# Kernel tuning notes

Hardware: AMD Instinct MI355X
Metric: run time of the kernel (lower is better)

## Reference

```python
import jax, jax.numpy as jnp
import numpy as np

N_E = 1024
N_H = 16
SZ = N_E // N_H  # 64
NEG_INF = float('-inf')


def _layernorm(x, g, b):
    # Faithful to source: unbiased variance (ddof=1), eps added AFTER sqrt.
    mu = jnp.mean(x, axis=-1, keepdims=True)
    v = jnp.var(x, axis=-1, keepdims=True, ddof=1)
    xn = (x - mu) / (jnp.sqrt(v) + 1e-8)
    return g * xn + b


def setup_inputs() -> dict:
    key = jax.random.key(0)
    ks = jax.random.split(key, 16)
    s = 0.02
    x = jax.random.normal(ks[0], (4, 2048, N_E), dtype=jnp.float32)
    # Stacked per-head Q/K/V linears: weight [H, sz, n_e], bias [H, sz]
    Wq = jax.random.normal(ks[1], (N_H, SZ, N_E), dtype=jnp.float32) * s
    bq = jax.random.normal(ks[2], (N_H, SZ), dtype=jnp.float32) * s
    Wk = jax.random.normal(ks[3], (N_H, SZ, N_E), dtype=jnp.float32) * s
    bk = jax.random.normal(ks[4], (N_H, SZ), dtype=jnp.float32) * s
    Wv = jax.random.normal(ks[5], (N_H, SZ, N_E), dtype=jnp.float32) * s
    bv = jax.random.normal(ks[6], (N_H, SZ), dtype=jnp.float32) * s
    Wo = jax.random.normal(ks[7], (N_E, N_E), dtype=jnp.float32) * s
    bo = jax.random.normal(ks[8], (N_E,), dtype=jnp.float32) * s
    g1 = jnp.ones((N_E,), dtype=jnp.float32)
    be1 = jnp.zeros((N_E,), dtype=jnp.float32)
    g2 = jnp.ones((N_E,), dtype=jnp.float32)
    be2 = jnp.zeros((N_E,), dtype=jnp.float32)
    W1 = jax.random.normal(ks[9], (4 * N_E, N_E), dtype=jnp.float32) * s
    bf1 = jax.random.normal(ks[10], (4 * N_E,), dtype=jnp.float32) * s
    W2 = jax.random.normal(ks[11], (N_E, 4 * N_E), dtype=jnp.float32) * s
    bf2 = jax.random.normal(ks[12], (N_E,), dtype=jnp.float32) * s
    return dict(x=x, Wq=Wq, bq=bq, Wk=Wk, bk=bk, Wv=Wv, bv=bv, Wo=Wo, bo=bo,
                g1=g1, be1=be1, g2=g2, be2=be2, W1=W1, bf1=bf1, W2=W2, bf2=bf2)


def reference(x, Wq, bq, Wk, bk, Wv, bv, Wo, bo, g1, be1, g2, be2, W1, bf1, W2, bf2):
    # --- MHA sublayer ---
    xn = _layernorm(x, g1, be1)
    # Q/K/V for all heads at once: [B, H, S, sz]
    Q = jnp.einsum('bsd,hkd->bhsk', xn, Wq) + bq[None, :, None, :]
    K = jnp.einsum('bsd,hkd->bhsk', xn, Wk) + bk[None, :, None, :]
    V = jnp.einsum('bsd,hkd->bhsk', xn, Wv) + bv[None, :, None, :]
    scores = jnp.einsum('bhqk,bhmk->bhqm', Q, K) / (SZ ** 0.5)  # [B,H,S,S]
    # Faithful to source quirk: mask where tril(scores) == 0
    masked = jnp.where(jnp.tril(scores) == 0, NEG_INF, scores)
    attn = jax.nn.softmax(masked, axis=-1)
    o = jnp.einsum('bhqm,bhmk->bhqk', attn, V)  # [B,H,S,sz]
    B, H, S, _ = o.shape
    o = jnp.transpose(o, (0, 2, 1, 3)).reshape(B, S, H * SZ)  # concat heads
    x = x + o @ Wo.T + bo
    # --- FFN sublayer (dropout = identity in eval) ---
    xn2 = _layernorm(x, g2, be2)
    h = jax.nn.gelu(xn2 @ W1.T + bf1, approximate=False)
    x = x + h @ W2.T + bf2
    return x
```

## Files before the change

### kernel.cpp

```cpp
#include <hip/hip_runtime.h>
#include <math.h>


typedef unsigned short u16;
typedef unsigned int u32;
typedef __attribute__((ext_vector_type(8))) short bf16x8;
typedef __attribute__((ext_vector_type(4))) float f32x4;

#define T_TOK 8192
#define DM    1024
#define SEQ   2048
#define PST   88
#define TST   136

__device__ __forceinline__ u16 f2bf(float f) {
  union { float f; unsigned int u; } c; c.f = f;
  unsigned int u = c.u + 0x7fffu + ((c.u >> 16) & 1u);
  return (u16)(u >> 16);
}

__device__ __forceinline__ u32 pk2(float a, float b) {
  return (u32)f2bf(a) | ((u32)f2bf(b) << 16);
}

__device__ __forceinline__ float bf2f(short s) {
  union { float f; unsigned int u; } c; c.u = ((u32)(u16)s) << 16;
  return c.f;
}

__device__ __forceinline__ void gload16(const void* gp, void* lp) {
  __builtin_amdgcn_global_load_lds(
      (const __attribute__((address_space(1))) void*)gp,
      (__attribute__((address_space(3))) void*)lp, 16, 0, 0);
}

__device__ __forceinline__ float gelu_tanh(float v) {
  float u = 0.7978845608f * (v + 0.044715f * v * v * v);
  return v / (1.0f + __expf(-2.0f * u));
}

__global__ __launch_bounds__(256) void prep_kernel(
    const float* __restrict__ x, const float* __restrict__ g,
    const float* __restrict__ b, u16* __restrict__ xnB,
    const float* __restrict__ Wq, const float* __restrict__ Wk,
    const float* __restrict__ Wv, const float* __restrict__ Wo,
    const float* __restrict__ W1, const float* __restrict__ W2,
    u16* __restrict__ WqkvB, u16* __restrict__ WoB,
    u16* __restrict__ W1B, u16* __restrict__ W2B,
    const float* __restrict__ bq, const float* __restrict__ bk,
    const float* __restrict__ bv, float* __restrict__ bqkv) {
  __shared__ float red[4];
  const int bid = blockIdx.x, tid = threadIdx.x;
  if (bid < 8192) {
    const int l = tid & 63, w = tid >> 6;
    const size_t row = bid;
    float4 v = reinterpret_cast<const float4*>(x + row * DM)[tid];
    float s = v.x + v.y + v.z + v.w;
#pragma unroll
    for (int off = 1; off < 64; off <<= 1) s += __shfl_xor(s, off, 64);
    if (l == 0) red[w] = s;
    __syncthreads();
    float mu = (red[0] + red[1] + red[2] + red[3]) * (1.0f / 1024.0f);
    float dx = v.x - mu, dy = v.y - mu, dz = v.z - mu, dw = v.w - mu;
    float ss = dx * dx + dy * dy + dz * dz + dw * dw;
#pragma unroll
    for (int off = 1; off < 64; off <<= 1) ss += __shfl_xor(ss, off, 64);
    __syncthreads();
    if (l == 0) red[w] = ss;
    __syncthreads();
    float var = (red[0] + red[1] + red[2] + red[3]) * (1.0f / 1023.0f);
    float inv = 1.0f / (sqrtf(var) + 1e-8f);
    const int c = tid * 4;
    u16* o = xnB + row * DM + c;
    o[0] = f2bf(dx * inv * g[c + 0] + b[c + 0]);
    o[1] = f2bf(dy * inv * g[c + 1] + b[c + 1]);
    o[2] = f2bf(dz * inv * g[c + 2] + b[c + 2]);
    o[3] = f2bf(dw * inv * g[c + 3] + b[c + 3]);
  } else if (bid < 10240) {
    for (int i = (bid - 8192) * 256 + tid; i < 3145728; i += 2048 * 256) {
      const float* s; u16* d; int j;
      if (i < 262144)       { s = Wq; d = WqkvB;           j = i; }
      else if (i < 524288)  { s = Wk; d = WqkvB + 1048576; j = i - 262144; }
      else if (i < 786432)  { s = Wv; d = WqkvB + 2097152; j = i - 524288; }
      else if (i < 1048576) { s = Wo; d = WoB;             j = i - 786432; }
      else if (i < 2097152) { s = W1; d = W1B;             j = i - 1048576; }
      else                  { s = W2; d = W2B;             j = i - 2097152; }
      float4 v = reinterpret_cast<const float4*>(s)[j];
      ushort4 o = { f2bf(v.x), f2bf(v.y), f2bf(v.z), f2bf(v.w) };
      reinterpret_cast<ushort4*>(d)[j] = o;
    }
  } else {
    int i = (bid - 10240) * 256 + tid;
    float val = (i < 1024) ? bq[i] : (i < 2048) ? bk[i - 1024] : bv[i - 2048];
    bqkv[i] = val;
  }
}

__global__ __launch_bounds__(256) void ln_kernel(const float* __restrict__ x,
    const float* __restrict__ g, const float* __restrict__ b, u16* __restrict__ out) {
  __shared__ float red[4];
  const int tid = threadIdx.x, l = tid & 63, w = tid >> 6;
  const size_t row = blockIdx.x;
  float4 v = reinterpret_cast<const float4*>(x + row * DM)[tid];
  float s = v.x + v.y + v.z + v.w;
#pragma unroll
  for (int off = 1; off < 64; off <<= 1) s += __shfl_xor(s, off, 64);
  if (l == 0) red[w] = s;
  __syncthreads();
  float mu = (red[0] + red[1] + red[2] + red[3]) * (1.0f / 1024.0f);
  float dx = v.x - mu, dy = v.y - mu, dz = v.z - mu, dw = v.w - mu;
  float ss = dx * dx + dy * dy + dz * dz + dw * dw;
#pragma unroll
  for (int off = 1; off < 64; off <<= 1) ss += __shfl_xor(ss, off, 64);
  __syncthreads();
  if (l == 0) red[w] = ss;
  __syncthreads();
  float var = (red[0] + red[1] + red[2] + red[3]) * (1.0f / 1023.0f);
  float inv = 1.0f / (sqrtf(var) + 1e-8f);
  const int c = tid * 4;
  u16* o = out + row * DM + c;
  o[0] = f2bf(dx * inv * g[c + 0] + b[c + 0]);
  o[1] = f2bf(dy * inv * g[c + 1] + b[c + 1]);
  o[2] = f2bf(dz * inv * g[c + 2] + b[c + 2]);
  o[3] = f2bf(dw * inv * g[c + 3] + b[c + 3]);
}

template <int EPI, int BM>
__global__ __launch_bounds__(512) void gemm8p(const u16* __restrict__ A,
    const u16* __restrict__ Bw, const float* __restrict__ bias,
    const float* res, void* Cout, void* aux, int M, int N, int K, int gx) {
  constexpr int MI  = BM / 32;
  constexpr int AMI = MI / 2;
  constexpr int VC  = (BM == 256) ? 6 : 5;
  __shared__ __align__(16) u16 shm[BM * 128 + 256 * 128];
  const int tid = threadIdx.x;
  const int l = tid & 63;
  const int w = tid >> 6;
  const int wm = w >> 2, wn = w & 3;
  const int lr = l & 15, lg = l >> 4;

  const int nb = gridDim.x;
  const int q = nb >> 3, r = nb & 7;
  const int xcd = blockIdx.x & 7, jj = blockIdx.x >> 3;
  const int lid = (xcd < r ? xcd * (q + 1) : r * (q + 1) + (xcd - r) * q) + jj;
  const int stid = lid >> 5, pos = lid & 31;
  const int nstx = gx >> 2;
  const int stx = stid % nstx, sty = stid / nstx;
  const int bx = stx * 4 + (pos & 3), by = sty * 8 + (pos >> 2);
  const int m0 = by * BM, n0 = bx * 256;

  const int Dl = tid * 16;
  const int Ls = Dl ^ (((Dl >> 7) & 3) << 4);
  const int srow = Ls >> 6;
  const int scol = (Ls & 63) >> 1;
  const u16* aS0 = A  + (size_t)(m0 + srow) * K + scol;
  const u16* aS1 = aS0 + (size_t)128 * K;
  const u16* bS0 = Bw + (size_t)(n0 + srow) * K + scol;
  const u16* bS1 = bS0 + (size_t)128 * K;

  const int sx = ((lr >> 1) & 3) << 4;
  const int aBase = (wm * (BM / 2) + lr) * 64 + ((lg * 16) ^ sx);
  const int bBase = (wn * 64 + lr) * 64 + ((lg * 16) ^ sx);

  f32x4 acc[MI][4];
#pragma unroll
  for (int i = 0; i < MI; ++i)
#pragma unroll
    for (int j = 0; j < 4; ++j) acc[i][j] = f32x4{0.f, 0.f, 0.f, 0.f};
  bf16x8 bv[2][4];

  const int NT = K >> 6;
  const int NI = NT >> 1;

  auto stA = [&](int d, int ks, int tile) {
    u16* dst = shm + (d * 2 + ks) * (BM * 32) + tid * 8;
    const int ko = tile * 64 + ks * 32;
    gload16(aS0 + ko, dst);
    if constexpr (BM == 256) gload16(aS1 + ko, dst + 4096);
  };
  auto stB = [&](int d, int ks, int tile) {
    u16* dst = shm + BM * 128 + (d * 2 + ks) * (256 * 32) + tid * 8;
    const int ko = tile * 64 + ks * 32;
    gload16(bS0 + ko, dst);
    gload16(bS1 + ko, dst + 4096);
  };

  stB(0, 0, 0); stB(0, 1, 0); stA(0, 0, 0); stA(0, 1, 0);
  stB(1, 0, 1); stB(1, 1, 1); stA(1, 0, 1);
  asm volatile("s_waitcnt vmcnt(%0)" :: "i"(VC) : "memory");
  __builtin_amdgcn_sched_barrier(0);
  __builtin_amdgcn_s_barrier();

#define PHASE(DBUF, KS, MH, READB, STAGE, ENDV)                               \
  {                                                                           \
    const char* abuf = (const char*)(shm + ((DBUF) * 2 + (KS)) * (BM * 32));  \
    const char* bbuf =                                                        \
        (const char*)(shm + BM * 128 + ((DBUF) * 2 + (KS)) * (256 * 32));     \
    bf16x8 av[AMI];                                                           \
    _Pragma("unroll")                                                         \
    for (int i = 0; i < AMI; ++i)                                             \
      av[i] = *(const bf16x8*)(abuf + aBase + ((MH) * AMI + i) * 1024);       \
    if (READB) {                                                              \
      _Pragma("unroll")                                                       \
      for (int ni = 0; ni < 4; ++ni)                                          \
        bv[KS][ni] = *(const bf16x8*)(bbuf + bBase + ni * 1024);              \
    }                                                                         \
    STAGE;                                                                    \
    __builtin_amdgcn_s_barrier();                                             \
    asm volatile("s_waitcnt lgkmcnt(0)" ::: "memory");                        \
    __builtin_amdgcn_sched_barrier(0);                                        \
    __builtin_amdgcn_s_setprio(1);                                            \
    _Pragma("unroll")                                                         \
    for (int i = 0; i < AMI; ++i)                                             \
      _Pragma("unroll")                                                       \
      for (int ni = 0; ni < 4; ++ni)                                          \
        acc[(MH) * AMI + i][ni] = __builtin_amdgcn_mfma_f32_16x16x32_bf16(    \
            av[i], bv[KS][ni], acc[(MH) * AMI + i][ni], 0, 0, 0);             \
    __builtin_amdgcn_s_setprio(0);                                            \
    ENDV;                                                                     \
    __builtin_amdgcn_s_barrier();                                             \
  }

#define ENDV_CNT                                                              \
  {                                                                           \
    if (t + 1 < NI) {                                                         \
      asm volatile("s_waitcnt vmcnt(%0)" :: "i"(VC) : "memory");              \
    } else {                                                                  \
      asm volatile("s_waitcnt vmcnt(0)" ::: "memory");                        \
    }                                                                         \
    __builtin_amdgcn_sched_barrier(0);                                        \
  }

  for (int t = 0; t < NI; ++t) {
    const int t2 = 2 * t;
    const bool s0 = (t2 + 2 < NT);
    const bool s1 = (t2 + 3 < NT);
    PHASE(0, 0, 0, 1, { stA(1, 1, t2 + 1); }, {});
    PHASE(0, 1, 0, 1, { if (s0) stB(0, 0, t2 + 2); }, {});
    PHASE(0, 0, 1, 0, { if (s0) stB(0, 1, t2 + 2); }, {});
    PHASE(0, 1, 1, 0, { if (s0) stA(0, 0, t2 + 2); }, ENDV_CNT);
    PHASE(1, 0, 0, 1, { if (s0) stA(0, 1, t2 + 2); }, {});
    PHASE(1, 1, 0, 1, { if (s1) stB(1, 0, t2 + 3); }, {});
    PHASE(1, 0, 1, 0, { if (s1) stB(1, 1, t2 + 3); }, {});
    PHASE(1, 1, 1, 0, { if (s1) stA(1, 0, t2 + 3); }, ENDV_CNT);
  }
#undef PHASE
#undef ENDV_CNT

  float bs[4];
#pragma unroll
  for (int ni = 0; ni < 4; ++ni) bs[ni] = bias[n0 + wn * 64 + ni * 16 + lr];

  if constexpr (EPI == 0) {
    if (n0 >= 2048) {
      u16* ldsT = shm;
#pragma unroll
      for (int mi = 0; mi < MI; ++mi)
#pragma unroll
        for (int ni = 0; ni < 4; ++ni) {
          const int c = wn * 64 + ni * 16 + lr;
          const int r0 = wm * (BM / 2) + mi * 16 + lg * 4;
          ushort4 pk = { f2bf(acc[mi][ni][0] + bs[ni]),
                         f2bf(acc[mi][ni][1] + bs[ni]),
                         f2bf(acc[mi][ni][2] + bs[ni]),
                         f2bf(acc[mi][ni][3] + bs[ni]) };
          *(ushort4*)&ldsT[c * TST + r0] = pk;
        }
      __syncthreads();
      const int b0 = m0 >> 11, s0b = m0 & 2047;
      const int cc = tid >> 1, hf = tid & 1;
      const int hd = (n0 - 2048) + cc, hh = hd >> 6, dd = hd & 63;
      u16* dst = (u16*)aux +
                 (((size_t)(b0 * 16 + hh) * 64 + dd) << 11) + s0b + hf * 64;
      const u16* srcT = &ldsT[cc * TST + hf * 64];
#pragma unroll
      for (int i2 = 0; i2 < 8; ++i2)
        *(bf16x8*)(dst + i2 * 8) = *(const bf16x8*)(srcT + i2 * 8);
      return;
    }
  }

#pragma unroll
  for (int mi = 0; mi < MI; ++mi) {
#pragma unroll
    for (int j = 0; j < 4; ++j) {
      const int rr = m0 + wm * (BM / 2) + mi * 16 + lg * 4 + j;
#pragma unroll
      for (int ni = 0; ni < 4; ++ni) {
        const int c = n0 + wn * 64 + ni * 16 + lr;
        float v = acc[mi][ni][j] + bs[ni];
        if constexpr (EPI == 0) {
          ((u16*)Cout)[(size_t)rr * 2048 + c] = f2bf(v);
        } else if constexpr (EPI == 1) {
          const size_t idx = (size_t)rr * N + c;
          ((float*)Cout)[idx] = v + res[idx];
        } else {
          const size_t idx = (size_t)rr * N + c;
          ((u16*)Cout)[idx] = f2bf(gelu_tanh(v));
        }
      }
    }
  }
}

__global__ __launch_bounds__(512) void attn_kernel(const u16* __restrict__ qk,
    const u16* __restrict__ vt, u16* __restrict__ obuf) {
  __shared__ __align__(16) u16 ldsK[3][64 * 64];
  __shared__ __align__(16) u16 ldsV[3][64 * 64];
  __shared__ __align__(16) u16 ldsP[8][2][16 * PST];
  const int tid = threadIdx.x, l = tid & 63, w = tid >> 6;
  const int lr = l & 15, lg = l >> 4;
  const int lid = (blockIdx.x & 7) * 32 + (blockIdx.x >> 3);
  const int bh = lid >> 2, bx = lid & 3;
  const int b = bh >> 4, h = bh & 15;
  const u16* qbase = qk + (size_t)b * SEQ * 2048 + h * 64;
  const u16* kbase = qk + (size_t)b * SEQ * 2048 + 1024 + h * 64;
  const u16* vbase = vt + (size_t)bh * 64 * SEQ;

  const int srow = tid >> 3;
  const int scb  = ((tid & 7) * 16) ^ ((srow & 7) << 4);
  const int sel  = scb >> 1;

  auto stageKV = [&](int t) {
    const int bi = t % 3;
    gload16(kbase + (size_t)(t * 64 + srow) * 2048 + sel, &ldsK[bi][tid * 8]);
    gload16(vbase + (size_t)srow * SEQ + t * 64 + sel,    &ldsV[bi][tid * 8]);
  };

#pragma unroll
  for (int half = 0; half < 2; ++half) {
    const int qt = half ? (7 - bx) : bx;
    const int q0 = qt * 256 + w * 32;
    bf16x8 qf[2][2];
#pragma unroll
    for (int mi = 0; mi < 2; ++mi)
#pragma unroll
      for (int ks = 0; ks < 2; ++ks) {
        bf16x8 raw = *(const bf16x8*)(qbase +
            (size_t)(q0 + mi * 16 + lr) * 2048 + ks * 32 + lg * 8);
        bf16x8 sc8;
#pragma unroll
        for (int i = 0; i < 8; ++i) sc8[i] = (short)f2bf(bf2f(raw[i]) * 0.125f);
        qf[mi][ks] = sc8;
      }

    f32x4 o[2][4];
#pragma unroll
    for (int mi = 0; mi < 2; ++mi)
#pragma unroll
      for (int nd = 0; nd < 4; ++nd) o[mi][nd] = f32x4{0.f, 0.f, 0.f, 0.f};
    float m_[2] = {-1e30f, -1e30f}, ls[2] = {0.f, 0.f};

    const int nt = 4 * qt + 4;
    const int qmaxw = q0 + 31;

    stageKV(0);

    for (int kt = 0; kt < nt; ++kt) {
      if (kt + 1 < nt) {
        stageKV(kt + 1);
        asm volatile("s_waitcnt vmcnt(2)" ::: "memory");
      } else {
        asm volatile("s_waitcnt vmcnt(0)" ::: "memory");
      }
      __builtin_amdgcn_s_barrier();
      __builtin_amdgcn_sched_barrier(0);
      const u16* bK = &ldsK[kt % 3][0];
      const u16* bV = &ldsV[kt % 3][0];

      if (kt * 64 <= qmaxw) {
        f32x4 sc[2][4];
#pragma unroll
        for (int mi = 0; mi < 2; ++mi)
#pragma unroll
          for (int ni = 0; ni < 4; ++ni) sc[mi][ni] = f32x4{0.f, 0.f, 0.f, 0.f};
#pragma unroll
        for (int ks = 0; ks < 2; ++ks)
#pragma unroll
          for (int ni = 0; ni < 4; ++ni) {
            const int r2 = ni * 16 + lr;
            const int cb = (r2 << 7) + ((ks * 64 + lg * 16) ^ ((r2 & 7) << 4));
            bf16x8 kf = *(const bf16x8*)&bK[cb >> 1];
            sc[0][ni] = __builtin_amdgcn_mfma_f32_16x16x32_bf16(kf, qf[0][ks], sc[0][ni], 0, 0, 0);
            sc[1][ni] = __builtin_amdgcn_mfma_f32_16x16x32_bf16(kf, qf[1][ks], sc[1][ni], 0, 0, 0);
          }

        if (kt * 64 + 63 > q0) {
#pragma unroll
          for (int mi = 0; mi < 2; ++mi) {
            const int qa = q0 + mi * 16 + lr;
#pragma unroll
            for (int ni = 0; ni < 4; ++ni)
#pragma unroll
              for (int j = 0; j < 4; ++j) {
                const int ka = kt * 64 + ni * 16 + lg * 4 + j;
                if (ka > qa) sc[mi][ni][j] = -1e30f;
              }
          }
        }

#pragma unroll
        for (int mi = 0; mi < 2; ++mi) {
          float mx = sc[mi][0][0];
#pragma unroll
          for (int ni = 0; ni < 4; ++ni)
#pragma unroll
            for (int j = 0; j < 4; ++j) mx = fmaxf(mx, sc[mi][ni][j]);
          mx = fmaxf(mx, __shfl_xor(mx, 16, 64));
          mx = fmaxf(mx, __shfl_xor(mx, 32, 64));
          if (!__all(mx <= m_[mi] + 8.0f)) {
            const float newm = fmaxf(m_[mi], mx);
            const float alpha = __expf(m_[mi] - newm);
            m_[mi] = newm;
            ls[mi] *= alpha;
#pragma unroll
            for (int nd = 0; nd < 4; ++nd) {
              o[mi][nd][0] *= alpha; o[mi][nd][1] *= alpha;
              o[mi][nd][2] *= alpha; o[mi][nd][3] *= alpha;
            }
          }
          float ps = 0.f;
#pragma unroll
          for (int ni = 0; ni < 4; ++ni) {
            float p0 = __expf(sc[mi][ni][0] - m_[mi]);
            float p1 = __expf(sc[mi][ni][1] - m_[mi]);
            float p2 = __expf(sc[mi][ni][2] - m_[mi]);
            float p3 = __expf(sc[mi][ni][3] - m_[mi]);
            ps += (p0 + p1) + (p2 + p3);
            u32 w0 = pk2(p0, p1), w1 = pk2(p2, p3);
            *(uint2*)&ldsP[w][mi][lr * PST + ni * 16 + lg * 4] = make_uint2(w0, w1);
          }
          ps += __shfl_xor(ps, 16, 64);
          ps += __shfl_xor(ps, 32, 64);
          ls[mi] += ps;
        }

#pragma unroll
        for (int ks = 0; ks < 2; ++ks) {
          bf16x8 pf0 = *(const bf16x8*)&ldsP[w][0][lr * PST + ks * 32 + lg * 8];
          bf16x8 pf1 = *(const bf16x8*)&ldsP[w][1][lr * PST + ks * 32 + lg * 8];
#pragma unroll
          for (int nd = 0; nd < 4; ++nd) {
            const int r2 = nd * 16 + lr;
            const int cb = (r2 << 7) + ((ks * 64 + lg * 16) ^ ((r2 & 7) << 4));
            bf16x8 vf = *(const bf16x8*)&bV[cb >> 1];
            o[0][nd] = __builtin_amdgcn_mfma_f32_16x16x32_bf16(vf, pf0, o[0][nd], 0, 0, 0);
            o[1][nd] = __builtin_amdgcn_mfma_f32_16x16x32_bf16(vf, pf1, o[1][nd], 0, 0, 0);
          }
        }
      }
    }
    __builtin_amdgcn_s_barrier();

#pragma unroll
    for (int mi = 0; mi < 2; ++mi) {
      const float inv = 1.0f / ls[mi];
      const int qrow = q0 + mi * 16 + lr;
      u16* op = obuf + (size_t)(b * SEQ + qrow) * DM + h * 64 + lg * 4;
#pragma unroll
      for (int nd = 0; nd < 4; ++nd) {
        ushort4 pk = { f2bf(o[mi][nd][0] * inv), f2bf(o[mi][nd][1] * inv),
                       f2bf(o[mi][nd][2] * inv), f2bf(o[mi][nd][3] * inv) };
        *(ushort4*)(op + nd * 16) = pk;
      }
    }
  }
}

extern "C" void kernel_launch(void* const* d_in, const int* in_sizes, int n_in,
                              void* d_out, int out_size, void* d_ws, size_t ws_size,
                              hipStream_t stream) {
  const float* x   = (const float*)d_in[0];
  const float* Wq  = (const float*)d_in[1];
  const float* bq  = (const float*)d_in[2];
  const float* Wk  = (const float*)d_in[3];
  const float* bk  = (const float*)d_in[4];
  const float* Wv  = (const float*)d_in[5];
  const float* bv  = (const float*)d_in[6];
  const float* Wo  = (const float*)d_in[7];
  const float* bo  = (const float*)d_in[8];
  const float* g1  = (const float*)d_in[9];
  const float* be1 = (const float*)d_in[10];
  const float* g2  = (const float*)d_in[11];
  const float* be2 = (const float*)d_in[12];
  const float* W1  = (const float*)d_in[13];
  const float* bf1 = (const float*)d_in[14];
  const float* W2  = (const float*)d_in[15];
  const float* bf2 = (const float*)d_in[16];
  float* out = (float*)d_out;

  char* ws = (char*)d_ws;
  size_t off = 0;
  auto alloc = [&](size_t bytes) {
    char* p = ws + off;
    off += (bytes + 255) & ~(size_t)255;
    return p;
  };
  u16* xnB = (u16*)alloc((size_t)T_TOK * DM * 2);
  u16* D    = (u16*)alloc((size_t)T_TOK * 4096 * 2);
  u16* qkB  = D;
  u16* VTg  = D + (size_t)T_TOK * 2048;
  u16* oB   = D + (size_t)T_TOK * 3072;
  u16* HB   = D;
  u16*   WqkvB = (u16*)alloc((size_t)3072 * 1024 * 2);
  u16*   WoB   = (u16*)alloc((size_t)1024 * 1024 * 2);
  u16*   W1B   = (u16*)alloc((size_t)4096 * 1024 * 2);
  u16*   W2B   = (u16*)alloc((size_t)1024 * 4096 * 2);
  float* bqkv  = (float*)alloc(3072 * 4);

  prep_kernel<<<10252, 256, 0, stream>>>(x, g1, be1, xnB,
                                         Wq, Wk, Wv, Wo, W1, W2,
                                         WqkvB, WoB, W1B, W2B,
                                         bq, bk, bv, bqkv);

  gemm8p<0, 128><<<768, 512, 0, stream>>>(xnB, WqkvB, bqkv, nullptr,
                                          qkB, VTg, T_TOK, 3072, 1024, 12);
  attn_kernel<<<256, 512, 0, stream>>>(qkB, VTg, oB);
  gemm8p<1, 128><<<256, 512, 0, stream>>>(oB, WoB, bo, x,
                                          out, nullptr, T_TOK, 1024, 1024, 4);

  ln_kernel<<<T_TOK, 256, 0, stream>>>(out, g2, be2, xnB);
  gemm8p<2, 256><<<512, 512, 0, stream>>>(xnB, W1B, bf1, nullptr,
                                          HB, nullptr, T_TOK, 4096, 1024, 16);
  gemm8p<1, 128><<<256, 512, 0, stream>>>(HB, W2B, bf2, out,
                                          out, nullptr, T_TOK, 1024, 4096, 4);
}
```

Before: 362.8 us.

## Restructure GEMM LDS staging to full 64-wide K tiles with coarser loads

Changes the shared-memory layout of the bf16 GEMM from two 32-column K halves per buffer to single 128-byte rows covering the full 64-wide K tile. A new XOR swizzle keeps LDS reads conflict-free, and the K-half is selected by XOR on the read address. Global-to-LDS staging now issues whole A or B tiles in fewer phases, with a fixed vmcnt wait, instead of splitting loads across all eight phases. The aim is more contiguous 128-byte global reads and simpler pipelining. The trade-off is burstier load issue, which may reduce overlap with the MFMA work.

After: 367.0 us. No clear change (+1.2%).

```diff
diff --git a/kernel.cpp b/kernel.cpp
--- a/kernel.cpp
+++ b/kernel.cpp
@@ -131,8 +131,8 @@
     const float* res, void* Cout, void* aux, int M, int N, int K, int gx) {
   constexpr int MI  = BM / 32;
   constexpr int AMI = MI / 2;
-  constexpr int VC  = (BM == 256) ? 6 : 5;
-  __shared__ __align__(16) u16 shm[BM * 128 + 256 * 128];
+  constexpr int LA4 = BM / 64;
+  __shared__ __align__(16) u16 shm[2 * BM * 64 + 2 * 256 * 64];
   const int tid = threadIdx.x;
   const int l = tid & 63;
   const int w = tid >> 6;
@@ -149,18 +149,14 @@
   const int bx = stx * 4 + (pos & 3), by = sty * 8 + (pos >> 2);
   const int m0 = by * BM, n0 = bx * 256;
 
-  const int Dl = tid * 16;
-  const int Ls = Dl ^ (((Dl >> 7) & 3) << 4);
-  const int srow = Ls >> 6;
-  const int scol = (Ls & 63) >> 1;
-  const u16* aS0 = A  + (size_t)(m0 + srow) * K + scol;
-  const u16* aS1 = aS0 + (size_t)128 * K;
-  const u16* bS0 = Bw + (size_t)(n0 + srow) * K + scol;
-  const u16* bS1 = bS0 + (size_t)128 * K;
-
-  const int sx = ((lr >> 1) & 3) << 4;
-  const int aBase = (wm * (BM / 2) + lr) * 64 + ((lg * 16) ^ sx);
-  const int bBase = (wn * 64 + lr) * 64 + ((lg * 16) ^ sx);
+  const int trow  = tid >> 3;
+  const int scolE = ((((tid & 7) * 16) ^ ((trow & 7) << 4)) >> 1);
+  const u16* aS0 = A  + (size_t)(m0 + trow) * K + scolE;
+  const u16* bS0 = Bw + (size_t)(n0 + trow) * K + scolE;
+
+  const int sx = (lr & 7) << 4;
+  const int aBase = (wm * (BM / 2) + lr) * 128 + ((lg * 16) ^ sx);
+  const int bBase = (wn * 64 + lr) * 128 + ((lg * 16) ^ sx);
 
   f32x4 acc[MI][4];
 #pragma unroll
@@ -172,38 +168,40 @@
   const int NT = K >> 6;
   const int NI = NT >> 1;
 
-  auto stA = [&](int d, int ks, int tile) {
-    u16* dst = shm + (d * 2 + ks) * (BM * 32) + tid * 8;
-    const int ko = tile * 64 + ks * 32;
-    gload16(aS0 + ko, dst);
-    if constexpr (BM == 256) gload16(aS1 + ko, dst + 4096);
+  auto stA = [&](int d, int tile) {
+    u16* dst = shm + d * (BM * 64) + tid * 8;
+    const u16* src = aS0 + tile * 64;
+#pragma unroll
+    for (int p = 0; p < LA4; ++p)
+      gload16(src + (size_t)p * 64 * K, dst + p * 4096);
   };
-  auto stB = [&](int d, int ks, int tile) {
-    u16* dst = shm + BM * 128 + (d * 2 + ks) * (256 * 32) + tid * 8;
-    const int ko = tile * 64 + ks * 32;
-    gload16(bS0 + ko, dst);
-    gload16(bS1 + ko, dst + 4096);
+  auto stB = [&](int d, int tile) {
+    u16* dst = shm + 2 * BM * 64 + d * (256 * 64) + tid * 8;
+    const u16* src = bS0 + tile * 64;
+#pragma unroll
+    for (int p = 0; p < 4; ++p)
+      gload16(src + (size_t)p * 64 * K, dst + p * 4096);
   };
 
-  stB(0, 0, 0); stB(0, 1, 0); stA(0, 0, 0); stA(0, 1, 0);
-  stB(1, 0, 1); stB(1, 1, 1); stA(1, 0, 1);
-  asm volatile("s_waitcnt vmcnt(%0)" :: "i"(VC) : "memory");
+  stB(0, 0); stA(0, 0); stB(1, 1);
+  asm volatile("s_waitcnt vmcnt(4)" ::: "memory");
   __builtin_amdgcn_sched_barrier(0);
   __builtin_amdgcn_s_barrier();
 
 #define PHASE(DBUF, KS, MH, READB, STAGE, ENDV)                               \
   {                                                                           \
-    const char* abuf = (const char*)(shm + ((DBUF) * 2 + (KS)) * (BM * 32));  \
-    const char* bbuf =                                                        \
-        (const char*)(shm + BM * 128 + ((DBUF) * 2 + (KS)) * (256 * 32));     \
+    const char* abuf = (const char*)(shm + (DBUF) * (BM * 64));               \
+    const char* bbuf = (const char*)(shm + 2 * BM * 64 + (DBUF) * (256 * 64));\
     bf16x8 av[AMI];                                                           \
     _Pragma("unroll")                                                         \
     for (int i = 0; i < AMI; ++i)                                             \
-      av[i] = *(const bf16x8*)(abuf + aBase + ((MH) * AMI + i) * 1024);       \
+      av[i] = *(const bf16x8*)(abuf + (aBase ^ ((KS) * 64)) +                 \
+                               ((MH) * AMI + i) * 2048);                      \
     if (READB) {                                                              \
       _Pragma("unroll")                                                       \
       for (int ni = 0; ni < 4; ++ni)                                          \
-        bv[KS][ni] = *(const bf16x8*)(bbuf + bBase + ni * 1024);              \
+        bv[KS][ni] = *(const bf16x8*)(bbuf + (bBase ^ ((KS) * 64)) +          \
+                                      ni * 2048);                             \
     }                                                                         \
     STAGE;                                                                    \
     __builtin_amdgcn_s_barrier();                                             \
@@ -224,7 +222,7 @@
 #define ENDV_CNT                                                              \
   {                                                                           \
     if (t + 1 < NI) {                                                         \
-      asm volatile("s_waitcnt vmcnt(%0)" :: "i"(VC) : "memory");              \
+      asm volatile("s_waitcnt vmcnt(4)" ::: "memory");                        \
     } else {                                                                  \
       asm volatile("s_waitcnt vmcnt(0)" ::: "memory");                        \
     }                                                                         \
@@ -235,14 +233,14 @@
     const int t2 = 2 * t;
     const bool s0 = (t2 + 2 < NT);
     const bool s1 = (t2 + 3 < NT);
-    PHASE(0, 0, 0, 1, { stA(1, 1, t2 + 1); }, {});
-    PHASE(0, 1, 0, 1, { if (s0) stB(0, 0, t2 + 2); }, {});
-    PHASE(0, 0, 1, 0, { if (s0) stB(0, 1, t2 + 2); }, {});
-    PHASE(0, 1, 1, 0, { if (s0) stA(0, 0, t2 + 2); }, ENDV_CNT);
-    PHASE(1, 0, 0, 1, { if (s0) stA(0, 1, t2 + 2); }, {});
-    PHASE(1, 1, 0, 1, { if (s1) stB(1, 0, t2 + 3); }, {});
-    PHASE(1, 0, 1, 0, { if (s1) stB(1, 1, t2 + 3); }, {});
-    PHASE(1, 1, 1, 0, { if (s1) stA(1, 0, t2 + 3); }, ENDV_CNT);
+    PHASE(0, 0, 0, 1, { stA(1, t2 + 1); }, {});
+    PHASE(0, 1, 0, 1, {}, {});
+    PHASE(0, 0, 1, 0, { if (s0) stB(0, t2 + 2); }, {});
+    PHASE(0, 1, 1, 0, {}, ENDV_CNT);
+    PHASE(1, 0, 0, 1, { if (s0) stA(0, t2 + 2); }, {});
+    PHASE(1, 1, 0, 1, {}, {});
+    PHASE(1, 0, 1, 0, { if (s1) stB(1, t2 + 3); }, {});
+    PHASE(1, 1, 1, 0, {}, ENDV_CNT);
   }
 #undef PHASE
 #undef ENDV_CNT
```

## Switch GEMMs to 128x128 tiles with 256-thread blocks and new swizzle

Applied to the files above, without the earlier changes.

Replaces the 128x256 and 256x256 block tiles (512 threads, 8 waves) with a uniform 128x128 tile run by 256 threads (4 waves in a 2x2 layout), each wave still computing 64x64. The LDS footprint per block shrinks and the grid doubles or quadruples, which should allow more blocks per CU and better load balance across the 256 CUs. The global-to-LDS staging mapping and the XOR swizzle are rewritten for 64-row slabs. Each block now reuses less data, so global and L2 traffic per FLOP rises, and the QKV transpose epilogue now covers a 128-column tile.

Measured after the change: 363.9 us. About the same (+0.3%).

```diff
diff --git a/kernel.cpp b/kernel.cpp
--- a/kernel.cpp
+++ b/kernel.cpp
@@ -125,18 +125,15 @@
   o[3] = f2bf(dw * inv * g[c + 3] + b[c + 3]);
 }
 
-template <int EPI, int BM>
-__global__ __launch_bounds__(512) void gemm8p(const u16* __restrict__ A,
+template <int EPI>
+__global__ __launch_bounds__(256) void gemm8p(const u16* __restrict__ A,
     const u16* __restrict__ Bw, const float* __restrict__ bias,
     const float* res, void* Cout, void* aux, int M, int N, int K, int gx) {
-  constexpr int MI  = BM / 32;
-  constexpr int AMI = MI / 2;
-  constexpr int VC  = (BM == 256) ? 6 : 5;
-  __shared__ __align__(16) u16 shm[BM * 128 + 256 * 128];
+  __shared__ __align__(16) u16 shm[8 * 4096];
   const int tid = threadIdx.x;
   const int l = tid & 63;
   const int w = tid >> 6;
-  const int wm = w >> 2, wn = w & 3;
+  const int wm = w >> 1, wn = w & 1;
   const int lr = l & 15, lg = l >> 4;
 
   const int nb = gridDim.x;
@@ -147,24 +144,22 @@
   const int nstx = gx >> 2;
   const int stx = stid % nstx, sty = stid / nstx;
   const int bx = stx * 4 + (pos & 3), by = sty * 8 + (pos >> 2);
-  const int m0 = by * BM, n0 = bx * 256;
-
-  const int Dl = tid * 16;
-  const int Ls = Dl ^ (((Dl >> 7) & 3) << 4);
-  const int srow = Ls >> 6;
-  const int scol = (Ls & 63) >> 1;
-  const u16* aS0 = A  + (size_t)(m0 + srow) * K + scol;
-  const u16* aS1 = aS0 + (size_t)128 * K;
-  const u16* bS0 = Bw + (size_t)(n0 + srow) * K + scol;
-  const u16* bS1 = bS0 + (size_t)128 * K;
-
-  const int sx = ((lr >> 1) & 3) << 4;
-  const int aBase = (wm * (BM / 2) + lr) * 64 + ((lg * 16) ^ sx);
+  const int m0 = by * 128, n0 = bx * 128;
+
+  const int srow  = tid >> 2;
+  const int scolE = ((((tid & 3) << 4) ^ ((srow & 6) << 3)) >> 1);
+  const u16* aS0 = A  + (size_t)(m0 + srow) * K + scolE;
+  const u16* aS1 = aS0 + (size_t)64 * K;
+  const u16* bS0 = Bw + (size_t)(n0 + srow) * K + scolE;
+  const u16* bS1 = bS0 + (size_t)64 * K;
+
+  const int sx = (lr & 6) << 3;
+  const int aBase = (wm * 64 + lr) * 64 + ((lg * 16) ^ sx);
   const int bBase = (wn * 64 + lr) * 64 + ((lg * 16) ^ sx);
 
-  f32x4 acc[MI][4];
-#pragma unroll
-  for (int i = 0; i < MI; ++i)
+  f32x4 acc[4][4];
+#pragma unroll
+  for (int i = 0; i < 4; ++i)
 #pragma unroll
     for (int j = 0; j < 4; ++j) acc[i][j] = f32x4{0.f, 0.f, 0.f, 0.f};
   bf16x8 bv[2][4];
@@ -173,33 +168,32 @@
   const int NI = NT >> 1;
 
   auto stA = [&](int d, int ks, int tile) {
-    u16* dst = shm + (d * 2 + ks) * (BM * 32) + tid * 8;
+    u16* dst = shm + (d * 2 + ks) * 4096 + tid * 8;
     const int ko = tile * 64 + ks * 32;
     gload16(aS0 + ko, dst);
-    if constexpr (BM == 256) gload16(aS1 + ko, dst + 4096);
+    gload16(aS1 + ko, dst + 2048);
   };
   auto stB = [&](int d, int ks, int tile) {
-    u16* dst = shm + BM * 128 + (d * 2 + ks) * (256 * 32) + tid * 8;
+    u16* dst = shm + 4 * 4096 + (d * 2 + ks) * 4096 + tid * 8;
     const int ko = tile * 64 + ks * 32;
     gload16(bS0 + ko, dst);
-    gload16(bS1 + ko, dst + 4096);
+    gload16(bS1 + ko, dst + 2048);
   };
 
   stB(0, 0, 0); stB(0, 1, 0); stA(0, 0, 0); stA(0, 1, 0);
   stB(1, 0, 1); stB(1, 1, 1); stA(1, 0, 1);
-  asm volatile("s_waitcnt vmcnt(%0)" :: "i"(VC) : "memory");
+  asm volatile("s_waitcnt vmcnt(6)" ::: "memory");
   __builtin_amdgcn_sched_barrier(0);
   __builtin_amdgcn_s_barrier();
 
 #define PHASE(DBUF, KS, MH, READB, STAGE, ENDV)                               \
   {                                                                           \
-    const char* abuf = (const char*)(shm + ((DBUF) * 2 + (KS)) * (BM * 32));  \
-    const char* bbuf =                                                        \
-        (const char*)(shm + BM * 128 + ((DBUF) * 2 + (KS)) * (256 * 32));     \
-    bf16x8 av[AMI];                                                           \
+    const char* abuf = (const char*)(shm + ((DBUF) * 2 + (KS)) * 4096);       \
+    const char* bbuf = (const char*)(shm + (4 + (DBUF) * 2 + (KS)) * 4096);   \
+    bf16x8 av[2];                                                             \
     _Pragma("unroll")                                                         \
-    for (int i = 0; i < AMI; ++i)                                             \
-      av[i] = *(const bf16x8*)(abuf + aBase + ((MH) * AMI + i) * 1024);       \
+    for (int i = 0; i < 2; ++i)                                               \
+      av[i] = *(const bf16x8*)(abuf + aBase + ((MH) * 2 + i) * 1024);         \
     if (READB) {                                                              \
       _Pragma("unroll")                                                       \
       for (int ni = 0; ni < 4; ++ni)                                          \
@@ -211,11 +205,11 @@
     __builtin_amdgcn_sched_barrier(0);                                        \
     __builtin_amdgcn_s_setprio(1);                                            \
     _Pragma("unroll")                                                         \
-    for (int i = 0; i < AMI; ++i)                                             \
+    for (int i = 0; i < 2; ++i)                                               \
       _Pragma("unroll")                                                       \
       for (int ni = 0; ni < 4; ++ni)                                          \
-        acc[(MH) * AMI + i][ni] = __builtin_amdgcn_mfma_f32_16x16x32_bf16(    \
-            av[i], bv[KS][ni], acc[(MH) * AMI + i][ni], 0, 0, 0);             \
+        acc[(MH) * 2 + i][ni] = __builtin_amdgcn_mfma_f32_16x16x32_bf16(      \
+            av[i], bv[KS][ni], acc[(MH) * 2 + i][ni], 0, 0, 0);               \
     __builtin_amdgcn_s_setprio(0);                                            \
     ENDV;                                                                     \
     __builtin_amdgcn_s_barrier();                                             \
@@ -224,7 +218,7 @@
 #define ENDV_CNT                                                              \
   {                                                                           \
     if (t + 1 < NI) {                                                         \
-      asm volatile("s_waitcnt vmcnt(%0)" :: "i"(VC) : "memory");              \
+      asm volatile("s_waitcnt vmcnt(6)" ::: "memory");                        \
     } else {                                                                  \
       asm volatile("s_waitcnt vmcnt(0)" ::: "memory");                        \
     }                                                                         \
@@ -255,11 +249,11 @@
     if (n0 >= 2048) {
       u16* ldsT = shm;
 #pragma unroll
-      for (int mi = 0; mi < MI; ++mi)
+      for (int mi = 0; mi < 4; ++mi)
 #pragma unroll
         for (int ni = 0; ni < 4; ++ni) {
           const int c = wn * 64 + ni * 16 + lr;
-          const int r0 = wm * (BM / 2) + mi * 16 + lg * 4;
+          const int r0 = wm * 64 + mi * 16 + lg * 4;
           ushort4 pk = { f2bf(acc[mi][ni][0] + bs[ni]),
                          f2bf(acc[mi][ni][1] + bs[ni]),
                          f2bf(acc[mi][ni][2] + bs[ni]),
@@ -281,10 +275,10 @@
   }
 
 #pragma unroll
-  for (int mi = 0; mi < MI; ++mi) {
+  for (int mi = 0; mi < 4; ++mi) {
 #pragma unroll
     for (int j = 0; j < 4; ++j) {
-      const int rr = m0 + wm * (BM / 2) + mi * 16 + lg * 4 + j;
+      const int rr = m0 + wm * 64 + mi * 16 + lg * 4 + j;
 #pragma unroll
       for (int ni = 0; ni < 4; ++ni) {
         const int c = n0 + wn * 64 + ni * 16 + lr;
@@ -513,15 +507,15 @@
                                          WqkvB, WoB, W1B, W2B,
                                          bq, bk, bv, bqkv);
 
-  gemm8p<0, 128><<<768, 512, 0, stream>>>(xnB, WqkvB, bqkv, nullptr,
-                                          qkB, VTg, T_TOK, 3072, 1024, 12);
+  gemm8p<0><<<1536, 256, 0, stream>>>(xnB, WqkvB, bqkv, nullptr,
+                                      qkB, VTg, T_TOK, 3072, 1024, 24);
   attn_kernel<<<256, 512, 0, stream>>>(qkB, VTg, oB);
-  gemm8p<1, 128><<<256, 512, 0, stream>>>(oB, WoB, bo, x,
-                                          out, nullptr, T_TOK, 1024, 1024, 4);
+  gemm8p<1><<<512, 256, 0, stream>>>(oB, WoB, bo, x,
+                                     out, nullptr, T_TOK, 1024, 1024, 8);
 
   ln_kernel<<<T_TOK, 256, 0, stream>>>(out, g2, be2, xnB);
-  gemm8p<2, 256><<<512, 512, 0, stream>>>(xnB, W1B, bf1, nullptr,
-                                          HB, nullptr, T_TOK, 4096, 1024, 16);
-  gemm8p<1, 128><<<256, 512, 0, stream>>>(HB, W2B, bf2, out,
-                                          out, nullptr, T_TOK, 1024, 4096, 4);
-}
+  gemm8p<2><<<2048, 256, 0, stream>>>(xnB, W1B, bf1, nullptr,
+                                      HB, nullptr, T_TOK, 4096, 1024, 32);
+  gemm8p<1><<<512, 256, 0, stream>>>(HB, W2B, bf2, out,
+                                     out, nullptr, T_TOK, 1024, 4096, 8);
+}
```
